# Kernel optimization log

Measured on AMD Instinct MI355X. Metric: run time of the kernel, lower is better.

The kernel has to match this reference:

```python
import jax, jax.numpy as jnp
import numpy as np

N = 50000
E = 800000
F = 64
HID = 64
HEADS = 4
NTYPES = 3


def layer_norm(x, g, b, eps=1e-5):
    mu = x.mean(-1, keepdims=True)
    var = ((x - mu) ** 2).mean(-1, keepdims=True)
    return (x - mu) * jax.lax.rsqrt(var + eps) * g + b


def gat_conv(x, src, dst, n, W, att_src, att_dst, bias, concat):
    # PyG GATConv: per-head linear transform, additive attention, segment softmax over dst.
    H, C = att_src.shape
    xp = (x @ W).reshape(n, H, C)                       # [N,H,C]
    a_s = (xp * att_src).sum(-1)                         # [N,H]
    a_d = (xp * att_dst).sum(-1)                         # [N,H]
    e = jax.nn.leaky_relu(a_s[src] + a_d[dst], 0.2)      # [Etot,H]
    m = jax.ops.segment_max(e, dst, num_segments=n)      # stable softmax per target
    ex = jnp.exp(e - m[dst])
    denom = jax.ops.segment_sum(ex, dst, num_segments=n)
    alpha = ex / (denom[dst] + 1e-16)                    # [Etot,H]
    msg = xp[src] * alpha[:, :, None]                    # [Etot,H,C]
    out = jax.ops.segment_sum(msg, dst, num_segments=n)  # [N,H,C]
    out = out.reshape(n, H * C) if concat else out.mean(1)
    return out + bias


def setup_inputs() -> dict:
    key = jax.random.key(0)
    ks = jax.random.split(key, 12)
    f32 = jnp.float32
    return {
        'node_features': jax.random.normal(ks[0], (N, F), f32),
        'node_types': jax.random.randint(ks[1], (N,), 0, NTYPES),
        'edge_index': jax.random.randint(ks[2], (2, E), 0, N),
        'type_emb': jax.random.normal(ks[3], (NTYPES, HID), f32) * 0.02,
        'proj_W': jax.random.normal(ks[4], (F, HID), f32) / np.sqrt(F).astype(np.float32),
        'proj_b': jnp.zeros((HID,), f32),
        'W0': jax.random.normal(ks[5], (HID, HEADS * HID), f32) / np.sqrt(HID).astype(np.float32),
        'att_src0': jax.random.normal(ks[6], (HEADS, HID), f32) * 0.1,
        'att_dst0': jax.random.normal(ks[7], (HEADS, HID), f32) * 0.1,
        'bias0': jnp.zeros((HEADS * HID,), f32),
        'ln0_g': jnp.ones((HEADS * HID,), f32),
        'ln0_b': jnp.zeros((HEADS * HID,), f32),
        'W1': jax.random.normal(ks[8], (HEADS * HID, HEADS * HID), f32) / np.sqrt(HEADS * HID).astype(np.float32),
        'att_src1': jax.random.normal(ks[9], (HEADS, HID), f32) * 0.1,
        'att_dst1': jax.random.normal(ks[10], (HEADS, HID), f32) * 0.1,
        'bias1': jnp.zeros((HID,), f32),
        'ln1_g': jnp.ones((HID,), f32),
        'ln1_b': jnp.zeros((HID,), f32),
    }


def reference(node_features, node_types, edge_index, type_emb, proj_W, proj_b,
              W0, att_src0, att_dst0, bias0, ln0_g, ln0_b,
              W1, att_src1, att_dst1, bias1, ln1_g, ln1_b):
    n = node_features.shape[0]
    loop = jnp.arange(n)
    src = jnp.concatenate([edge_index[0], loop])  # add_self_loops=True (PyG default)
    dst = jnp.concatenate([edge_index[1], loop])
    # input projection + node-type embedding
    x = node_features @ proj_W + proj_b + type_emb[node_types]
    # layer 0: concat heads -> [N, HEADS*HID]
    h = gat_conv(x, src, dst, n, W0, att_src0, att_dst0, bias0, True)
    h = jax.nn.relu(layer_norm(h, ln0_g, ln0_b))  # dropout is identity in eval
    # layer 1: mean over heads -> [N, HID]; residual skipped (shape mismatch 256 vs 64)
    h2 = gat_conv(h, src, dst, n, W1, att_src1, att_dst1, bias1, False)
    h2 = jax.nn.relu(layer_norm(h2, ln1_g, ln1_b))
    return h2
```

## Files before the change

kernel.cpp:

```cpp
#include <hip/hip_runtime.h>
#include <hip/hip_bf16.h>
#include <hip/hip_fp16.h>

typedef unsigned short u16;
typedef unsigned int u32;
typedef short s16x8 __attribute__((ext_vector_type(8)));
typedef float f32x4 __attribute__((ext_vector_type(4)));

__device__ __forceinline__ float bf2f(u16 u) {
  return __uint_as_float(((u32)u) << 16);
}

__device__ __forceinline__ u16 f2b(float f) {
  __hip_bfloat16 h = __float2bfloat16(f);
  return *(u16*)&h;
}

__device__ __forceinline__ u32 packbf(float lo, float hi) {
  return (u32)f2b(lo) | ((u32)f2b(hi) << 16);
}

__device__ __forceinline__ bool sniff_bf16(const void* ones) {
  u32 w = *(const u32*)ones;
  return (w >> 16) == (w & 0xFFFFu);
}

__device__ __forceinline__ float ldf(const void* p, size_t i, bool bf) {
  return bf ? bf2f(((const u16*)p)[i]) : ((const float*)p)[i];
}

__device__ __forceinline__ float rdlane_f(float v, int e) {
  return __uint_as_float((u32)__builtin_amdgcn_readlane((int)__float_as_uint(v), e));
}

__global__ void fill_f32(float* __restrict__ p, float v, size_t n) {
  size_t i = (size_t)blockIdx.x * blockDim.x + threadIdx.x;
  if (i < n) p[i] = v;
}

__global__ __launch_bounds__(256) void deg_count_k(const int* __restrict__ ei, int E, int N,
                                                   int* __restrict__ deg) {
  int i = blockIdx.x * 256 + threadIdx.x;
  if (i >= E + N) return;
  int d = (i < E) ? ei[E + i] : (i - E);
  atomicAdd(deg + d, 1);
}

__global__ __launch_bounds__(256) void scan_local_k(const int* __restrict__ deg,
                                                    int* __restrict__ off,
                                                    int* __restrict__ bsum, int N) {
  __shared__ int ps[256];
  int t = threadIdx.x;
  int i = blockIdx.x * 256 + t;
  int v = (i < N) ? deg[i] : 0;
  ps[t] = v;
  __syncthreads();
#pragma unroll
  for (int o = 1; o < 256; o <<= 1) {
    int u = (t >= o) ? ps[t - o] : 0;
    __syncthreads();
    ps[t] += u;
    __syncthreads();
  }
  if (i < N) off[i] = ps[t] - v;
  if (t == 255) bsum[blockIdx.x] = ps[255];
}

__global__ __launch_bounds__(1024) void scan_bsum_k(int* __restrict__ bsum, int nb) {
  __shared__ int ps[1024];
  int t = threadIdx.x;
  int v = (t < nb) ? bsum[t] : 0;
  ps[t] = v;
  __syncthreads();
#pragma unroll
  for (int o = 1; o < 1024; o <<= 1) {
    int u = (t >= o) ? ps[t - o] : 0;
    __syncthreads();
    ps[t] += u;
    __syncthreads();
  }
  if (t < nb) bsum[t] = ps[t] - v;
}

__global__ __launch_bounds__(256) void scan_add_k(int* __restrict__ off,
                                                  const int* __restrict__ bsum,
                                                  int* __restrict__ cur, int N, int Etot) {
  int i = blockIdx.x * 256 + threadIdx.x;
  if (i == 0) off[N] = Etot;
  if (i >= N) return;
  int o = off[i] + bsum[i >> 8];
  off[i] = o;
  cur[i] = o;
}

__global__ __launch_bounds__(256) void scatter_k(const int* __restrict__ ei, int E, int N,
                                                 int* __restrict__ cur, int* __restrict__ csr) {
  int i = blockIdx.x * 256 + threadIdx.x;
  if (i >= E + N) return;
  int s, d;
  if (i < E) { s = ei[i]; d = ei[E + i]; } else { s = i - E; d = s; }
  int p = atomicAdd(cur + d, 1);
  csr[p] = s;
}

__global__ __launch_bounds__(256) void wpack_k(const void* __restrict__ W,
                                               const void* __restrict__ ones,
                                               u16* __restrict__ Wp, int K) {
  bool bf = sniff_bf16(ones);
  int i = blockIdx.x * 256 + threadIdx.x;
  if (i >= K * 256) return;
  int j = i & 7;
  int q = (i >> 3) & 3;
  int c = (i >> 5) & 255;
  int kc = i >> 13;
  int k = kc * 32 + q * 8 + j;
  Wp[i] = f2b(ldf(W, (size_t)k * 256 + c, bf));
}

__global__ __launch_bounds__(256) void wpack64_k(const void* __restrict__ W,
                                                 const void* __restrict__ ones,
                                                 u16* __restrict__ Wp) {
  bool bf = sniff_bf16(ones);
  int i = blockIdx.x * 256 + threadIdx.x;
  if (i >= 64 * 64) return;
  int j = i & 7;
  int q = (i >> 3) & 3;
  int c = (i >> 5) & 63;
  int kc = i >> 11;
  int k = kc * 32 + q * 8 + j;
  Wp[i] = f2b(ldf(W, (size_t)k * 64 + c, bf));
}

__global__ __launch_bounds__(256) void attvec2_k(
    const void* __restrict__ W0, const void* __restrict__ atts,
    const void* __restrict__ attd, const void* __restrict__ pW,
    const void* __restrict__ pb, const void* __restrict__ temb,
    const void* __restrict__ ones, u16* __restrict__ Wpe, float* __restrict__ ca) {
  bool bf = sniff_bf16(ones);
  __shared__ float va[256], vd[256];
  int t = threadIdx.x;
  int h = t >> 6, k = t & 63;
  {
    float s = 0.f, d = 0.f;
    for (int c = 0; c < 64; c++) {
      float w = ldf(W0, (size_t)k * 256 + h * 64 + c, bf);
      s += w * ldf(atts, h * 64 + c, bf);
      d += w * ldf(attd, h * 64 + c, bf);
    }
    va[t] = s;
    vd[t] = d;
  }
  __syncthreads();
  {
    int i = k;
    float wa = 0.f, wd = 0.f;
    for (int kk = 0; kk < 64; kk++) {
      float wv = ldf(pW, (size_t)i * 64 + kk, bf);
      wa += wv * va[h * 64 + kk];
      wd += wv * vd[h * 64 + kk];
    }
    int kc = i >> 5, q = (i >> 3) & 3, j = i & 7;
    Wpe[((kc * 16 + h) * 4 + q) * 8 + j] = f2b(wa);
    Wpe[((kc * 16 + 4 + h) * 4 + q) * 8 + j] = f2b(wd);
  }
  Wpe[256 + t] = 0;
  Wpe[768 + t] = 0;
  if (t < 12) {
    int ty = t >> 2, hh = t & 3;
    float sa = 0.f, sd = 0.f;
    for (int kk = 0; kk < 64; kk++) {
      float bv = ldf(pb, kk, bf) + ldf(temb, ty * 64 + kk, bf);
      sa += bv * va[hh * 64 + kk];
      sd += bv * vd[hh * 64 + kk];
    }
    ca[t] = sa;
    ca[12 + t] = sd;
  }
}

__global__ __launch_bounds__(256) void proj2_k(
    const void* __restrict__ nf, const int* __restrict__ ntype,
    const u16* __restrict__ Wpp, const u16* __restrict__ Wpe,
    const void* __restrict__ pbias, const void* __restrict__ temb,
    const float* __restrict__ ca, const void* __restrict__ ones,
    u16* __restrict__ x, float* __restrict__ aS, float* __restrict__ aD, int N) {
  bool bf = sniff_bf16(ones);
  int t = threadIdx.x;
  int wave = t >> 6, lane = t & 63;
  int r = lane & 15, q = lane >> 4;
  int row0 = blockIdx.x * 16;
  int arow = row0 + r;
  if (arow >= N) arow = N - 1;
  f32x4 xacc = {0.f, 0.f, 0.f, 0.f};
  f32x4 eacc = {0.f, 0.f, 0.f, 0.f};
#pragma unroll
  for (int kc = 0; kc < 2; kc++) {
    s16x8 a;
    if (bf) {
      a = *(const s16x8*)((const u16*)nf + (size_t)arow * 64 + kc * 32 + q * 8);
    } else {
      const float* fp = (const float*)nf + (size_t)arow * 64 + kc * 32 + q * 8;
#pragma unroll
      for (int j = 0; j < 8; j++) a[j] = (short)f2b(fp[j]);
    }
    {
      int c = wave * 16 + r;
      s16x8 b = *(const s16x8*)(Wpp + (((size_t)kc * 64 + c) * 4 + q) * 8);
      xacc = __builtin_amdgcn_mfma_f32_16x16x32_bf16(a, b, xacc, 0, 0, 0);
    }
    if (wave == 3) {
      s16x8 b = *(const s16x8*)(Wpe + (((size_t)kc * 16 + r) * 4 + q) * 8);
      eacc = __builtin_amdgcn_mfma_f32_16x16x32_bf16(a, b, eacc, 0, 0, 0);
    }
  }
#pragma unroll
  for (int rg = 0; rg < 4; rg++) {
    int row = row0 + q * 4 + rg;
    if (row >= N) continue;
    int col = wave * 16 + r;
    int ty = ntype[row];
    float v = xacc[rg] + ldf(pbias, col, bf) + ldf(temb, ty * 64 + col, bf);
    x[(size_t)row * 64 + col] = f2b(v);
    if (wave == 3 && r < 8) {
      if (r < 4) aS[(size_t)row * 4 + r] = eacc[rg] + ca[ty * 4 + r];
      else       aD[(size_t)row * 4 + (r - 4)] = eacc[rg] + ca[12 + ty * 4 + (r - 4)];
    }
  }
}

__global__ __launch_bounds__(256) void agg0_k(
    const int* __restrict__ off, const int* __restrict__ csr,
    const float* __restrict__ aS, const float* __restrict__ aD,
    const u16* __restrict__ x, u16* __restrict__ Ag, int N) {
  int n = blockIdx.x * 4 + (threadIdx.x >> 6);
  int lane = threadIdx.x & 63;
  if (n >= N) return;
  int start = off[n], end = off[n + 1];
  float4 ad4 = *(const float4*)(aD + (size_t)n * 4);
  float ad[4] = {ad4.x, ad4.y, ad4.z, ad4.w};
  float den[4] = {0.f, 0.f, 0.f, 0.f};
  float acc[4] = {0.f, 0.f, 0.f, 0.f};
  const u16* xl = x + lane;

  for (int cs = start; cs < end; cs += 64) {
    int cnt = end - cs; if (cnt > 64) cnt = 64;
    int s = 0;
    float ex[4] = {0.f, 0.f, 0.f, 0.f};
    if (lane < cnt) {
      s = csr[cs + lane];
      float4 as4 = *(const float4*)(aS + (size_t)s * 4);
      float av[4] = {as4.x, as4.y, as4.z, as4.w};
#pragma unroll
      for (int h = 0; h < 4; h++) {
        float v = av[h] + ad[h];
        v = (v > 0.f ? v : 0.2f * v) - 3.0f;
        ex[h] = __expf(v);
        den[h] += ex[h];
      }
    }
#pragma unroll 8
    for (int e = 0; e < cnt; e++) {
      int se = __builtin_amdgcn_readlane(s, e);
      float w0 = rdlane_f(ex[0], e);
      float w1 = rdlane_f(ex[1], e);
      float w2 = rdlane_f(ex[2], e);
      float w3 = rdlane_f(ex[3], e);
      float xv = bf2f(xl[(size_t)se * 64]);
      acc[0] += w0 * xv;
      acc[1] += w1 * xv;
      acc[2] += w2 * xv;
      acc[3] += w3 * xv;
    }
  }
#pragma unroll
  for (int h = 0; h < 4; h++) {
#pragma unroll
    for (int o = 32; o > 0; o >>= 1) den[h] += __shfl_xor(den[h], o, 64);
    acc[h] /= (den[h] + 1e-16f);
  }
#pragma unroll
  for (int h = 0; h < 4; h++) Ag[(size_t)n * 256 + h * 64 + lane] = f2b(acc[h]);
}

__global__ __launch_bounds__(256) void l0g1_k(
    const u16* __restrict__ Ag, const u16* __restrict__ Wp0,
    const void* __restrict__ bias0, const void* __restrict__ g0,
    const void* __restrict__ be0, const u16* __restrict__ Wp1,
    const void* __restrict__ atts, const void* __restrict__ attd,
    const void* __restrict__ ones,
    u16* __restrict__ C, float* __restrict__ aS, float* __restrict__ aD, int N) {
  bool bf = sniff_bf16(ones);
  __shared__ u16 hs[16][264];
  __shared__ float sm_s[4][16], sm_q[4][16];
  int t = threadIdx.x;
  int wave = t >> 6, lane = t & 63;
  int r = lane & 15, q = lane >> 4;
  int row0 = blockIdx.x * 16;
  int arow = row0 + r;
  if (arow >= N) arow = N - 1;
  {
    const u16* ap = Ag + (size_t)arow * 256 + wave * 64 + q * 8;
    f32x4 acc[4] = {{0.f, 0.f, 0.f, 0.f}, {0.f, 0.f, 0.f, 0.f},
                    {0.f, 0.f, 0.f, 0.f}, {0.f, 0.f, 0.f, 0.f}};
#pragma unroll
    for (int kc = 0; kc < 2; kc++) {
      s16x8 a = *(const s16x8*)(ap + kc * 32);
#pragma unroll
      for (int ct = 0; ct < 4; ct++) {
        int c = wave * 64 + ct * 16 + r;
        s16x8 b = *(const s16x8*)(Wp0 + (((size_t)kc * 256 + c) * 4 + q) * 8);
        acc[ct] = __builtin_amdgcn_mfma_f32_16x16x32_bf16(a, b, acc[ct], 0, 0, 0);
      }
    }
    float yv[4][4];
    float s_p[4] = {0.f, 0.f, 0.f, 0.f};
    float q_p[4] = {0.f, 0.f, 0.f, 0.f};
#pragma unroll
    for (int ct = 0; ct < 4; ct++) {
      float bc = ldf(bias0, wave * 64 + ct * 16 + r, bf);
#pragma unroll
      for (int rg = 0; rg < 4; rg++) {
        float y = acc[ct][rg] + bc;
        yv[ct][rg] = y;
        s_p[rg] += y;
        q_p[rg] += y * y;
      }
    }
#pragma unroll
    for (int o = 1; o < 16; o <<= 1) {
#pragma unroll
      for (int rg = 0; rg < 4; rg++) {
        s_p[rg] += __shfl_xor(s_p[rg], o, 64);
        q_p[rg] += __shfl_xor(q_p[rg], o, 64);
      }
    }
    if (r == 0) {
#pragma unroll
      for (int rg = 0; rg < 4; rg++) {
        sm_s[wave][q * 4 + rg] = s_p[rg];
        sm_q[wave][q * 4 + rg] = q_p[rg];
      }
    }
    __syncthreads();
#pragma unroll
    for (int rg = 0; rg < 4; rg++) {
      int lr = q * 4 + rg;
      float mu = (sm_s[0][lr] + sm_s[1][lr] + sm_s[2][lr] + sm_s[3][lr]) * (1.f / 256.f);
      float vq = (sm_q[0][lr] + sm_q[1][lr] + sm_q[2][lr] + sm_q[3][lr]) * (1.f / 256.f) - mu * mu;
      float inv = rsqrtf(vq + 1e-5f);
#pragma unroll
      for (int ct = 0; ct < 4; ct++) {
        int c = wave * 64 + ct * 16 + r;
        float o_ = (yv[ct][rg] - mu) * inv * ldf(g0, c, bf) + ldf(be0, c, bf);
        hs[lr][c] = f2b(fmaxf(o_, 0.f));
      }
    }
  }
  __syncthreads();
  int colw = wave * 64;
  f32x4 acc[4] = {{0.f, 0.f, 0.f, 0.f}, {0.f, 0.f, 0.f, 0.f},
                  {0.f, 0.f, 0.f, 0.f}, {0.f, 0.f, 0.f, 0.f}};
#pragma unroll
  for (int kc = 0; kc < 8; kc++) {
    s16x8 a = *(const s16x8*)&hs[r][kc * 32 + q * 8];
#pragma unroll
    for (int ct = 0; ct < 4; ct++) {
      int c = colw + ct * 16 + r;
      s16x8 b = *(const s16x8*)(Wp1 + (((size_t)kc * 256 + c) * 4 + q) * 8);
      acc[ct] = __builtin_amdgcn_mfma_f32_16x16x32_bf16(a, b, acc[ct], 0, 0, 0);
    }
  }
#pragma unroll
  for (int ct = 0; ct < 4; ct++) {
#pragma unroll
    for (int rg = 0; rg < 4; rg++) {
      int row = row0 + q * 4 + rg;
      if (row < N) C[(size_t)row * 256 + colw + ct * 16 + r] = f2b(acc[ct][rg]);
    }
  }
  float sp[4] = {0.f, 0.f, 0.f, 0.f};
  float dp[4] = {0.f, 0.f, 0.f, 0.f};
#pragma unroll
  for (int ct = 0; ct < 4; ct++) {
    int c = colw + ct * 16 + r;
    float av = ldf(atts, c, bf);
    float dv = ldf(attd, c, bf);
#pragma unroll
    for (int rg = 0; rg < 4; rg++) {
      sp[rg] += acc[ct][rg] * av;
      dp[rg] += acc[ct][rg] * dv;
    }
  }
#pragma unroll
  for (int o = 1; o < 16; o <<= 1) {
#pragma unroll
    for (int rg = 0; rg < 4; rg++) {
      sp[rg] += __shfl_xor(sp[rg], o, 64);
      dp[rg] += __shfl_xor(dp[rg], o, 64);
    }
  }
  if (r == 0) {
#pragma unroll
    for (int rg = 0; rg < 4; rg++) {
      int row = row0 + q * 4 + rg;
      if (row < N) {
        aS[(size_t)row * 4 + wave] = sp[rg];
        aD[(size_t)row * 4 + wave] = dp[rg];
      }
    }
  }
}

__global__ __launch_bounds__(256) void agg1_k(
    const int* __restrict__ off, const int* __restrict__ csr,
    const float* __restrict__ aS, const float* __restrict__ aD,
    const u16* __restrict__ xp,
    const void* __restrict__ bias, const void* __restrict__ g,
    const void* __restrict__ b, void* __restrict__ out, int N) {
  bool bf = sniff_bf16(g);
  int n = blockIdx.x * 4 + (threadIdx.x >> 6);
  int lane = threadIdx.x & 63;
  if (n >= N) return;
  int start = off[n], end = off[n + 1];
  bool hiSel = (lane & 32) != 0;
  float4 ad4 = *(const float4*)(aD + (size_t)n * 4);
  float ad[4] = {ad4.x, ad4.y, ad4.z, ad4.w};
  float den[4] = {0.f, 0.f, 0.f, 0.f};
  float acc[4] = {0.f, 0.f, 0.f, 0.f};
  const u32* xp32 = (const u32*)xp;

  for (int cs = start; cs < end; cs += 64) {
    int cnt = end - cs; if (cnt > 64) cnt = 64;
    int s = 0;
    float ex[4] = {0.f, 0.f, 0.f, 0.f};
    if (lane < cnt) {
      s = csr[cs + lane];
      float4 as4 = *(const float4*)(aS + (size_t)s * 4);
      float av[4] = {as4.x, as4.y, as4.z, as4.w};
#pragma unroll
      for (int h = 0; h < 4; h++) {
        float v = av[h] + ad[h];
        v = (v > 0.f ? v : 0.2f * v) - 3.0f;
        ex[h] = __expf(v);
        den[h] += ex[h];
      }
    }
#pragma unroll 8
    for (int e = 0; e < cnt; e++) {
      int se = __builtin_amdgcn_readlane(s, e);
      float w0 = rdlane_f(ex[0], e);
      float w1 = rdlane_f(ex[1], e);
      float w2 = rdlane_f(ex[2], e);
      float w3 = rdlane_f(ex[3], e);
      float wA = hiSel ? w1 : w0;
      float wB = hiSel ? w3 : w2;
      const u32* xr = xp32 + (size_t)se * 128 + lane;
      u32 dA = xr[0];
      u32 dB = xr[64];
      acc[0] += wA * __uint_as_float(dA << 16);
      acc[1] += wA * __uint_as_float(dA & 0xffff0000u);
      acc[2] += wB * __uint_as_float(dB << 16);
      acc[3] += wB * __uint_as_float(dB & 0xffff0000u);
    }
  }
#pragma unroll
  for (int h = 0; h < 4; h++) {
#pragma unroll
    for (int o = 32; o > 0; o >>= 1) den[h] += __shfl_xor(den[h], o, 64);
  }
  {
    float dA = (hiSel ? den[1] : den[0]) + 1e-16f;
    float dB = (hiSel ? den[3] : den[2]) + 1e-16f;
    acc[0] /= dA; acc[1] /= dA;
    acc[2] /= dB; acc[3] /= dB;
  }
  float p0 = acc[0] + acc[2];
  float p1 = acc[1] + acc[3];
  p0 += __shfl_xor(p0, 32, 64);
  p1 += __shfl_xor(p1, 32, 64);
  int c = 2 * (lane & 31);
  float z0 = 0.25f * p0 + ldf(bias, c, bf);
  float z1 = 0.25f * p1 + ldf(bias, c + 1, bf);
  float sum = z0 + z1;
#pragma unroll
  for (int o = 32; o > 0; o >>= 1) sum += __shfl_xor(sum, o, 64);
  float mu = sum * (1.f / 128.f);
  float d0 = z0 - mu, d1 = z1 - mu;
  float sq = d0 * d0 + d1 * d1;
#pragma unroll
  for (int o = 32; o > 0; o >>= 1) sq += __shfl_xor(sq, o, 64);
  float inv = rsqrtf(sq * (1.f / 128.f) + 1e-5f);
  float y0 = fmaxf(d0 * inv * ldf(g, c, bf) + ldf(b, c, bf), 0.f);
  float y1 = fmaxf(d1 * inv * ldf(g, c + 1, bf) + ldf(b, c + 1, bf), 0.f);
  if (lane < 32) {
    if (bf) {
      ((u32*)out)[(size_t)n * 32 + lane] = packbf(y0, y1);
    } else {
      ((float2*)out)[(size_t)n * 32 + lane] = make_float2(y0, y1);
    }
  }
}

extern "C" void kernel_launch(void* const* d_in, const int* in_sizes, int n_in,
                              void* d_out, int out_size, void* d_ws, size_t ws_size,
                              hipStream_t stream) {
  const void* nf   = d_in[0];
  const int* ntyp  = (const int*)d_in[1];
  const int* ei    = (const int*)d_in[2];
  const void* temb = d_in[3];
  const void* pW   = d_in[4];
  const void* pb   = d_in[5];
  const void* W0   = d_in[6];
  const void* as0  = d_in[7];
  const void* ad0  = d_in[8];
  const void* b0   = d_in[9];
  const void* g0   = d_in[10];
  const void* be0  = d_in[11];
  const void* W1   = d_in[12];
  const void* as1  = d_in[13];
  const void* ad1  = d_in[14];
  const void* b1   = d_in[15];
  const void* g1   = d_in[16];
  const void* be1  = d_in[17];

  int N = in_sizes[0] / 64;
  int E = in_sizes[2] / 2;
  int Etot = E + N;

  u16* Wp0 = (u16*)d_ws;
  u16* Wp1 = Wp0 + 64 * 256;
  u16* Wpp = Wp1 + 256 * 256;
  u16* Wpe = Wpp + 64 * 64;
  u16* xb  = Wpe + 1024;
  u16* Ag  = xb + (size_t)N * 64;
  u16* A   = Ag + (size_t)N * 256;
  float* aS = (float*)(A + (size_t)N * 256);
  float* aD = aS + (size_t)N * 4;
  float* ca = aD + (size_t)N * 4;
  int* deg  = (int*)(ca + 32);
  int* off  = deg + N;
  int* csr  = off + N + 1;
  int* bsum = csr + Etot;

  dim3 b256(256);
  int nodeBlocks = (N + 3) / 4;
  int edgeBlocksT = (Etot + 255) / 256;
  int gemmBlocks = (N + 15) / 16;
  int scanBlocks = (N + 255) / 256;

  fill_f32<<<(N + 255) / 256, b256, 0, stream>>>((float*)deg, 0.f, (size_t)N);
  deg_count_k<<<edgeBlocksT, b256, 0, stream>>>(ei, E, N, deg);
  scan_local_k<<<scanBlocks, b256, 0, stream>>>(deg, off, bsum, N);
  scan_bsum_k<<<1, 1024, 0, stream>>>(bsum, scanBlocks);
  scan_add_k<<<scanBlocks, b256, 0, stream>>>(off, bsum, deg, N, Etot);
  scatter_k<<<edgeBlocksT, b256, 0, stream>>>(ei, E, N, deg, csr);
  wpack_k<<<(64 * 256 + 255) / 256, b256, 0, stream>>>(W0, g0, Wp0, 64);
  wpack_k<<<(256 * 256 + 255) / 256, b256, 0, stream>>>(W1, g0, Wp1, 256);
  wpack64_k<<<(64 * 64 + 255) / 256, b256, 0, stream>>>(pW, g0, Wpp);
  attvec2_k<<<1, b256, 0, stream>>>(W0, as0, ad0, pW, pb, temb, g0, Wpe, ca);

  proj2_k<<<gemmBlocks, b256, 0, stream>>>(nf, ntyp, Wpp, Wpe, pb, temb, ca, g0,
                                           xb, aS, aD, N);
  agg0_k<<<nodeBlocks, b256, 0, stream>>>(off, csr, aS, aD, xb, Ag, N);
  l0g1_k<<<gemmBlocks, b256, 0, stream>>>(Ag, Wp0, b0, g0, be0, Wp1, as1, ad1, g0,
                                          A, aS, aD, N);
  agg1_k<<<nodeBlocks, b256, 0, stream>>>(off, csr, aS, aD, A, b1, g1, be1, d_out, N);
}
```

Before: 414.9 us.

## Fuse layer-0 aggregation into GEMM kernel and merge prep/scan launches

The layer-0 edge aggregation is folded into the layer-0 GEMM/layer-1 projection kernel. Each block aggregates its 16 rows into shared memory and feeds them straight to MFMA, so the N×256 Ag intermediate never goes to global memory. The weight packing and attention-vector kernels are merged into one multi-role launch, and the bsum scan is replaced by a per-block reduction inside the add kernel. The memset becomes hipMemsetAsync. Layer-0 and layer-1 attention logits get separate buffers because the fused kernel reads one and writes the other. The risk is lower parallelism in the aggregation: each wave now processes 4 nodes serially before a block barrier, so load imbalance from varying degree can stall the GEMM.

```diff
diff --git a/kernel.cpp b/kernel.cpp
--- a/kernel.cpp
+++ b/kernel.cpp
@@ -31,11 +31,6 @@
 
 __device__ __forceinline__ float rdlane_f(float v, int e) {
   return __uint_as_float((u32)__builtin_amdgcn_readlane((int)__float_as_uint(v), e));
-}
-
-__global__ void fill_f32(float* __restrict__ p, float v, size_t n) {
-  size_t i = (size_t)blockIdx.x * blockDim.x + threadIdx.x;
-  if (i < n) p[i] = v;
 }
 
 __global__ __launch_bounds__(256) void deg_count_k(const int* __restrict__ ei, int E, int N,
@@ -66,31 +61,27 @@
   if (t == 255) bsum[blockIdx.x] = ps[255];
 }
 
-__global__ __launch_bounds__(1024) void scan_bsum_k(int* __restrict__ bsum, int nb) {
-  __shared__ int ps[1024];
+__global__ __launch_bounds__(256) void scan_add2_k(int* __restrict__ off,
+                                                   const int* __restrict__ bsum,
+                                                   int* __restrict__ cur,
+                                                   int N, int Etot, int nb) {
+  __shared__ int red[256];
   int t = threadIdx.x;
-  int v = (t < nb) ? bsum[t] : 0;
-  ps[t] = v;
+  int b = blockIdx.x;
+  red[t] = (t < nb && t < b) ? bsum[t] : 0;
   __syncthreads();
 #pragma unroll
-  for (int o = 1; o < 1024; o <<= 1) {
-    int u = (t >= o) ? ps[t - o] : 0;
+  for (int o = 128; o > 0; o >>= 1) {
+    if (t < o) red[t] += red[t + o];
     __syncthreads();
-    ps[t] += u;
-    __syncthreads();
-  }
-  if (t < nb) bsum[t] = ps[t] - v;
-}
-
-__global__ __launch_bounds__(256) void scan_add_k(int* __restrict__ off,
-                                                  const int* __restrict__ bsum,
-                                                  int* __restrict__ cur, int N, int Etot) {
-  int i = blockIdx.x * 256 + threadIdx.x;
+  }
+  int pre = red[0];
+  int i = b * 256 + t;
   if (i == 0) off[N] = Etot;
   if (i >= N) return;
-  int o = off[i] + bsum[i >> 8];
-  off[i] = o;
-  cur[i] = o;
+  int o2 = off[i] + pre;
+  off[i] = o2;
+  cur[i] = o2;
 }
 
 __global__ __launch_bounds__(256) void scatter_k(const int* __restrict__ ei, int E, int N,
@@ -103,78 +94,73 @@
   csr[p] = s;
 }
 
-__global__ __launch_bounds__(256) void wpack_k(const void* __restrict__ W,
-                                               const void* __restrict__ ones,
-                                               u16* __restrict__ Wp, int K) {
+__global__ __launch_bounds__(256) void prep_k(
+    const void* __restrict__ W0, const void* __restrict__ W1,
+    const void* __restrict__ pW, const void* __restrict__ atts,
+    const void* __restrict__ attd, const void* __restrict__ pb,
+    const void* __restrict__ temb, const void* __restrict__ ones,
+    u16* __restrict__ Wp0, u16* __restrict__ Wp1, u16* __restrict__ Wpp,
+    u16* __restrict__ Wpe, float* __restrict__ ca) {
   bool bf = sniff_bf16(ones);
-  int i = blockIdx.x * 256 + threadIdx.x;
-  if (i >= K * 256) return;
-  int j = i & 7;
-  int q = (i >> 3) & 3;
-  int c = (i >> 5) & 255;
-  int kc = i >> 13;
-  int k = kc * 32 + q * 8 + j;
-  Wp[i] = f2b(ldf(W, (size_t)k * 256 + c, bf));
-}
-
-__global__ __launch_bounds__(256) void wpack64_k(const void* __restrict__ W,
-                                                 const void* __restrict__ ones,
-                                                 u16* __restrict__ Wp) {
-  bool bf = sniff_bf16(ones);
-  int i = blockIdx.x * 256 + threadIdx.x;
-  if (i >= 64 * 64) return;
-  int j = i & 7;
-  int q = (i >> 3) & 3;
-  int c = (i >> 5) & 63;
-  int kc = i >> 11;
-  int k = kc * 32 + q * 8 + j;
-  Wp[i] = f2b(ldf(W, (size_t)k * 64 + c, bf));
-}
-
-__global__ __launch_bounds__(256) void attvec2_k(
-    const void* __restrict__ W0, const void* __restrict__ atts,
-    const void* __restrict__ attd, const void* __restrict__ pW,
-    const void* __restrict__ pb, const void* __restrict__ temb,
-    const void* __restrict__ ones, u16* __restrict__ Wpe, float* __restrict__ ca) {
-  bool bf = sniff_bf16(ones);
-  __shared__ float va[256], vd[256];
+  int b = blockIdx.x;
   int t = threadIdx.x;
-  int h = t >> 6, k = t & 63;
-  {
-    float s = 0.f, d = 0.f;
-    for (int c = 0; c < 64; c++) {
-      float w = ldf(W0, (size_t)k * 256 + h * 64 + c, bf);
-      s += w * ldf(atts, h * 64 + c, bf);
-      d += w * ldf(attd, h * 64 + c, bf);
-    }
-    va[t] = s;
-    vd[t] = d;
-  }
-  __syncthreads();
-  {
-    int i = k;
-    float wa = 0.f, wd = 0.f;
-    for (int kk = 0; kk < 64; kk++) {
-      float wv = ldf(pW, (size_t)i * 64 + kk, bf);
-      wa += wv * va[h * 64 + kk];
-      wd += wv * vd[h * 64 + kk];
-    }
-    int kc = i >> 5, q = (i >> 3) & 3, j = i & 7;
-    Wpe[((kc * 16 + h) * 4 + q) * 8 + j] = f2b(wa);
-    Wpe[((kc * 16 + 4 + h) * 4 + q) * 8 + j] = f2b(wd);
-  }
-  Wpe[256 + t] = 0;
-  Wpe[768 + t] = 0;
-  if (t < 12) {
-    int ty = t >> 2, hh = t & 3;
-    float sa = 0.f, sd = 0.f;
-    for (int kk = 0; kk < 64; kk++) {
-      float bv = ldf(pb, kk, bf) + ldf(temb, ty * 64 + kk, bf);
-      sa += bv * va[hh * 64 + kk];
-      sd += bv * vd[hh * 64 + kk];
-    }
-    ca[t] = sa;
-    ca[12 + t] = sd;
+  if (b < 320) {
+    const void* W = (b < 64) ? W0 : W1;
+    u16* Wp = (b < 64) ? Wp0 : Wp1;
+    int i = (b < 64 ? b : b - 64) * 256 + t;
+    int j = i & 7;
+    int q = (i >> 3) & 3;
+    int c = (i >> 5) & 255;
+    int kc = i >> 13;
+    int k = kc * 32 + q * 8 + j;
+    Wp[i] = f2b(ldf(W, (size_t)k * 256 + c, bf));
+  } else if (b < 336) {
+    int i = (b - 320) * 256 + t;
+    int j = i & 7;
+    int q = (i >> 3) & 3;
+    int c = (i >> 5) & 63;
+    int kc = i >> 11;
+    int k = kc * 32 + q * 8 + j;
+    Wpp[i] = f2b(ldf(pW, (size_t)k * 64 + c, bf));
+  } else {
+    __shared__ float va[256], vd[256];
+    int h = t >> 6, k = t & 63;
+    {
+      float s = 0.f, d = 0.f;
+      for (int c = 0; c < 64; c++) {
+        float w = ldf(W0, (size_t)k * 256 + h * 64 + c, bf);
+        s += w * ldf(atts, h * 64 + c, bf);
+        d += w * ldf(attd, h * 64 + c, bf);
+      }
+      va[t] = s;
+      vd[t] = d;
+    }
+    __syncthreads();
+    {
+      int i = k;
+      float wa = 0.f, wd = 0.f;
+      for (int kk = 0; kk < 64; kk++) {
+        float wv = ldf(pW, (size_t)i * 64 + kk, bf);
+        wa += wv * va[h * 64 + kk];
+        wd += wv * vd[h * 64 + kk];
+      }
+      int kc = i >> 5, q = (i >> 3) & 3, j = i & 7;
+      Wpe[((kc * 16 + h) * 4 + q) * 8 + j] = f2b(wa);
+      Wpe[((kc * 16 + 4 + h) * 4 + q) * 8 + j] = f2b(wd);
+    }
+    Wpe[256 + t] = 0;
+    Wpe[768 + t] = 0;
+    if (t < 12) {
+      int ty = t >> 2, hh = t & 3;
+      float sa = 0.f, sd = 0.f;
+      for (int kk = 0; kk < 64; kk++) {
+        float bv = ldf(pb, kk, bf) + ldf(temb, ty * 64 + kk, bf);
+        sa += bv * va[hh * 64 + kk];
+        sd += bv * vd[hh * 64 + kk];
+      }
+      ca[t] = sa;
+      ca[12 + t] = sd;
+    }
   }
 }
 
@@ -228,83 +214,80 @@
   }
 }
 
-__global__ __launch_bounds__(256) void agg0_k(
+__global__ __launch_bounds__(256) void l0g1f_k(
     const int* __restrict__ off, const int* __restrict__ csr,
-    const float* __restrict__ aS, const float* __restrict__ aD,
-    const u16* __restrict__ x, u16* __restrict__ Ag, int N) {
-  int n = blockIdx.x * 4 + (threadIdx.x >> 6);
-  int lane = threadIdx.x & 63;
-  if (n >= N) return;
-  int start = off[n], end = off[n + 1];
-  float4 ad4 = *(const float4*)(aD + (size_t)n * 4);
-  float ad[4] = {ad4.x, ad4.y, ad4.z, ad4.w};
-  float den[4] = {0.f, 0.f, 0.f, 0.f};
-  float acc[4] = {0.f, 0.f, 0.f, 0.f};
-  const u16* xl = x + lane;
-
-  for (int cs = start; cs < end; cs += 64) {
-    int cnt = end - cs; if (cnt > 64) cnt = 64;
-    int s = 0;
-    float ex[4] = {0.f, 0.f, 0.f, 0.f};
-    if (lane < cnt) {
-      s = csr[cs + lane];
-      float4 as4 = *(const float4*)(aS + (size_t)s * 4);
-      float av[4] = {as4.x, as4.y, as4.z, as4.w};
-#pragma unroll
-      for (int h = 0; h < 4; h++) {
-        float v = av[h] + ad[h];
-        v = (v > 0.f ? v : 0.2f * v) - 3.0f;
-        ex[h] = __expf(v);
-        den[h] += ex[h];
-      }
-    }
-#pragma unroll 8
-    for (int e = 0; e < cnt; e++) {
-      int se = __builtin_amdgcn_readlane(s, e);
-      float w0 = rdlane_f(ex[0], e);
-      float w1 = rdlane_f(ex[1], e);
-      float w2 = rdlane_f(ex[2], e);
-      float w3 = rdlane_f(ex[3], e);
-      float xv = bf2f(xl[(size_t)se * 64]);
-      acc[0] += w0 * xv;
-      acc[1] += w1 * xv;
-      acc[2] += w2 * xv;
-      acc[3] += w3 * xv;
-    }
-  }
-#pragma unroll
-  for (int h = 0; h < 4; h++) {
-#pragma unroll
-    for (int o = 32; o > 0; o >>= 1) den[h] += __shfl_xor(den[h], o, 64);
-    acc[h] /= (den[h] + 1e-16f);
-  }
-#pragma unroll
-  for (int h = 0; h < 4; h++) Ag[(size_t)n * 256 + h * 64 + lane] = f2b(acc[h]);
-}
-
-__global__ __launch_bounds__(256) void l0g1_k(
-    const u16* __restrict__ Ag, const u16* __restrict__ Wp0,
+    const float* __restrict__ aS0, const float* __restrict__ aD0,
+    const u16* __restrict__ x, const u16* __restrict__ Wp0,
     const void* __restrict__ bias0, const void* __restrict__ g0,
     const void* __restrict__ be0, const u16* __restrict__ Wp1,
     const void* __restrict__ atts, const void* __restrict__ attd,
     const void* __restrict__ ones,
-    u16* __restrict__ C, float* __restrict__ aS, float* __restrict__ aD, int N) {
+    u16* __restrict__ C, float* __restrict__ aS1, float* __restrict__ aD1, int N) {
   bool bf = sniff_bf16(ones);
+  __shared__ u16 ag[16][264];
   __shared__ u16 hs[16][264];
   __shared__ float sm_s[4][16], sm_q[4][16];
   int t = threadIdx.x;
   int wave = t >> 6, lane = t & 63;
   int r = lane & 15, q = lane >> 4;
   int row0 = blockIdx.x * 16;
-  int arow = row0 + r;
-  if (arow >= N) arow = N - 1;
+  const u16* xl = x + lane;
+  for (int jj = 0; jj < 4; jj++) {
+    int lr = wave * 4 + jj;
+    int n = row0 + lr;
+    float den[4] = {0.f, 0.f, 0.f, 0.f};
+    float acc[4] = {0.f, 0.f, 0.f, 0.f};
+    if (n < N) {
+      int start = off[n], end = off[n + 1];
+      float4 ad4 = *(const float4*)(aD0 + (size_t)n * 4);
+      float ad[4] = {ad4.x, ad4.y, ad4.z, ad4.w};
+      for (int cs = start; cs < end; cs += 64) {
+        int cnt = end - cs; if (cnt > 64) cnt = 64;
+        int s = 0;
+        float ex[4] = {0.f, 0.f, 0.f, 0.f};
+        if (lane < cnt) {
+          s = csr[cs + lane];
+          float4 as4 = *(const float4*)(aS0 + (size_t)s * 4);
+          float av[4] = {as4.x, as4.y, as4.z, as4.w};
+#pragma unroll
+          for (int h = 0; h < 4; h++) {
+            float v = av[h] + ad[h];
+            v = (v > 0.f ? v : 0.2f * v) - 3.0f;
+            ex[h] = __expf(v);
+            den[h] += ex[h];
+          }
+        }
+#pragma unroll 8
+        for (int e = 0; e < cnt; e++) {
+          int se = __builtin_amdgcn_readlane(s, e);
+          float w0 = rdlane_f(ex[0], e);
+          float w1 = rdlane_f(ex[1], e);
+          float w2 = rdlane_f(ex[2], e);
+          float w3 = rdlane_f(ex[3], e);
+          float xv = bf2f(xl[(size_t)se * 64]);
+          acc[0] += w0 * xv;
+          acc[1] += w1 * xv;
+          acc[2] += w2 * xv;
+          acc[3] += w3 * xv;
+        }
+      }
+#pragma unroll
+      for (int h = 0; h < 4; h++) {
+#pragma unroll
+        for (int o = 32; o > 0; o >>= 1) den[h] += __shfl_xor(den[h], o, 64);
+        acc[h] /= (den[h] + 1e-16f);
+      }
+    }
+#pragma unroll
+    for (int h = 0; h < 4; h++) ag[lr][h * 64 + lane] = f2b(acc[h]);
+  }
+  __syncthreads();
   {
-    const u16* ap = Ag + (size_t)arow * 256 + wave * 64 + q * 8;
     f32x4 acc[4] = {{0.f, 0.f, 0.f, 0.f}, {0.f, 0.f, 0.f, 0.f},
                     {0.f, 0.f, 0.f, 0.f}, {0.f, 0.f, 0.f, 0.f}};
 #pragma unroll
     for (int kc = 0; kc < 2; kc++) {
-      s16x8 a = *(const s16x8*)(ap + kc * 32);
+      s16x8 a = *(const s16x8*)&ag[r][wave * 64 + kc * 32 + q * 8];
 #pragma unroll
       for (int ct = 0; ct < 4; ct++) {
         int c = wave * 64 + ct * 16 + r;
@@ -404,8 +387,8 @@
     for (int rg = 0; rg < 4; rg++) {
       int row = row0 + q * 4 + rg;
       if (row < N) {
-        aS[(size_t)row * 4 + wave] = sp[rg];
-        aD[(size_t)row * 4 + wave] = dp[rg];
+        aS1[(size_t)row * 4 + wave] = sp[rg];
+        aD1[(size_t)row * 4 + wave] = dp[rg];
       }
     }
   }
@@ -532,11 +515,12 @@
   u16* Wpp = Wp1 + 256 * 256;
   u16* Wpe = Wpp + 64 * 64;
   u16* xb  = Wpe + 1024;
-  u16* Ag  = xb + (size_t)N * 64;
-  u16* A   = Ag + (size_t)N * 256;
-  float* aS = (float*)(A + (size_t)N * 256);
-  float* aD = aS + (size_t)N * 4;
-  float* ca = aD + (size_t)N * 4;
+  u16* A   = xb + (size_t)N * 64;
+  float* aS0b = (float*)(A + (size_t)N * 256);
+  float* aD0b = aS0b + (size_t)N * 4;
+  float* aS1b = aD0b + (size_t)N * 4;
+  float* aD1b = aS1b + (size_t)N * 4;
+  float* ca = aD1b + (size_t)N * 4;
   int* deg  = (int*)(ca + 32);
   int* off  = deg + N;
   int* csr  = off + N + 1;
@@ -548,21 +532,17 @@
   int gemmBlocks = (N + 15) / 16;
   int scanBlocks = (N + 255) / 256;
 
-  fill_f32<<<(N + 255) / 256, b256, 0, stream>>>((float*)deg, 0.f, (size_t)N);
+  hipMemsetAsync(deg, 0, (size_t)N * sizeof(int), stream);
   deg_count_k<<<edgeBlocksT, b256, 0, stream>>>(ei, E, N, deg);
   scan_local_k<<<scanBlocks, b256, 0, stream>>>(deg, off, bsum, N);
-  scan_bsum_k<<<1, 1024, 0, stream>>>(bsum, scanBlocks);
-  scan_add_k<<<scanBlocks, b256, 0, stream>>>(off, bsum, deg, N, Etot);
+  scan_add2_k<<<scanBlocks, b256, 0, stream>>>(off, bsum, deg, N, Etot, scanBlocks);
   scatter_k<<<edgeBlocksT, b256, 0, stream>>>(ei, E, N, deg, csr);
-  wpack_k<<<(64 * 256 + 255) / 256, b256, 0, stream>>>(W0, g0, Wp0, 64);
-  wpack_k<<<(256 * 256 + 255) / 256, b256, 0, stream>>>(W1, g0, Wp1, 256);
-  wpack64_k<<<(64 * 64 + 255) / 256, b256, 0, stream>>>(pW, g0, Wpp);
-  attvec2_k<<<1, b256, 0, stream>>>(W0, as0, ad0, pW, pb, temb, g0, Wpe, ca);
+  prep_k<<<337, b256, 0, stream>>>(W0, W1, pW, as0, ad0, pb, temb, g0,
+                                   Wp0, Wp1, Wpp, Wpe, ca);
 
   proj2_k<<<gemmBlocks, b256, 0, stream>>>(nf, ntyp, Wpp, Wpe, pb, temb, ca, g0,
-                                           xb, aS, aD, N);
-  agg0_k<<<nodeBlocks, b256, 0, stream>>>(off, csr, aS, aD, xb, Ag, N);
-  l0g1_k<<<gemmBlocks, b256, 0, stream>>>(Ag, Wp0, b0, g0, be0, Wp1, as1, ad1, g0,
-                                          A, aS, aD, N);
-  agg1_k<<<nodeBlocks, b256, 0, stream>>>(off, csr, aS, aD, A, b1, g1, be1, d_out, N);
-}
+                                           xb, aS0b, aD0b, N);
+  l0g1f_k<<<gemmBlocks, b256, 0, stream>>>(off, csr, aS0b, aD0b, xb, Wp0, b0, g0, be0,
+                                           Wp1, as1, ad1, g0, A, aS1b, aD1b, N);
+  agg1_k<<<nodeBlocks, b256, 0, stream>>>(off, csr, aS1b, aD1b, A, b1, g1, be1, d_out, N);
+}
```

New measurement: 429.3 us. +3.5%, slower.
